# Kernel optimization log

Hardware: AMD Instinct MI355X
Metric: run time of the kernel (lower is better)

Reference implementation:

```python
import jax, jax.numpy as jnp
import numpy as np

N = 10000      # num_nodes
E = 80000      # num_edges
IN = 256       # input_dim
T = 768        # text_embedding_dim
H1, H2 = 1024, 1024
HEADS = 4
ND = 100       # num_domains
NS = 10000     # num_skills
SD = 128       # skill_dim
B = 1024       # skill batch
K = 20         # skills per set
LN_EPS = 1e-5
COS_EPS = 1e-8
NEG_SLOPE = 0.2


def setup_inputs() -> dict:
    key = jax.random.key(0)
    ks = jax.random.split(key, 64)
    r = lambda i, shape, s=0.02: jax.random.normal(ks[i], shape, jnp.float32) * s
    inp = {}
    inp['x'] = jax.random.normal(ks[0], (N, IN), jnp.float32)
    inp['edge_index'] = jax.random.randint(ks[1], (2, E), 0, N)
    inp['domain_ids'] = jax.random.randint(ks[2], (N,), 0, ND)
    inp['skill_ids_1'] = jax.random.randint(ks[3], (B, K), 0, NS)
    inp['skill_ids_2'] = jax.random.randint(ks[4], (B, K), 0, NS)
    for j, name in enumerate(['bio', 'expertise', 'needs', 'goals']):
        inp[name + '_embeddings'] = jax.random.normal(ks[5 + j], (N, T), jnp.float32)
        inp[name + '_w'] = r(9 + 2 * j, (T, T))
        inp[name + '_b'] = jnp.zeros((T,), jnp.float32)
    dims = [IN + 4 * T, H1, H2]
    for i in range(2):
        din, dout = dims[i], dims[i + 1]
        base = 20 + 8 * i
        inp[f'gcn_w{i}'] = r(base, (din, dout))
        inp[f'gcn_b{i}'] = jnp.zeros((dout,), jnp.float32)
        inp[f'gat_w{i}'] = r(base + 1, (dout, dout))
        inp[f'gat_as{i}'] = r(base + 2, (HEADS, dout // HEADS), 0.1)
        inp[f'gat_ad{i}'] = r(base + 3, (HEADS, dout // HEADS), 0.1)
        inp[f'gat_b{i}'] = jnp.zeros((dout,), jnp.float32)
        inp[f'ln_g{i}'] = jnp.ones((dout,), jnp.float32)
        inp[f'ln_b{i}'] = jnp.zeros((dout,), jnp.float32)
    inp['dom_emb'] = r(40, (ND, H2), 1.0)
    inp['dom_w'] = r(41, (H2, H2))
    inp['dom_b'] = jnp.zeros((H2,), jnp.float32)
    inp['skill_emb'] = r(42, (NS, SD), 1.0)
    inp['c_w1'] = r(43, (2 * SD, H2))
    inp['c_b1'] = jnp.zeros((H2,), jnp.float32)
    inp['c_w2'] = r(44, (H2, 1))
    inp['c_b2'] = jnp.zeros((1,), jnp.float32)
    return inp


def _layernorm(x, g, b):
    m = x.mean(-1, keepdims=True)
    v = ((x - m) ** 2).mean(-1, keepdims=True)
    return (x - m) * jax.lax.rsqrt(v + LN_EPS) * g + b


def _gcn(x, src, dst, W, b, n):
    # PyG GCNConv: self loops already in (src,dst); symmetric normalization
    xw = x @ W
    deg = jnp.zeros((n,), x.dtype).at[dst].add(1.0)
    dinv = jax.lax.rsqrt(jnp.maximum(deg, 1.0))  # deg >= 1 due to self loops
    norm = dinv[src] * dinv[dst]                 # [Etot]
    out = jnp.zeros_like(xw).at[dst].add(norm[:, None] * xw[src])
    return out + b


def _gat(x, src, dst, W, a_s, a_d, b, n, heads):
    c = W.shape[1] // heads
    h = (x @ W).reshape(n, heads, c)             # [N,H,C]
    es = jnp.einsum('nhc,hc->nh', h, a_s)
    ed = jnp.einsum('nhc,hc->nh', h, a_d)
    e = jax.nn.leaky_relu(es[src] + ed[dst], NEG_SLOPE)   # [Etot,H]
    m = jnp.full((n, heads), -jnp.inf, x.dtype).at[dst].max(e)
    ee = jnp.exp(e - m[dst])
    s = jnp.zeros((n, heads), x.dtype).at[dst].add(ee)
    alpha = ee / s[dst]                          # segment softmax over dst
    out = jnp.zeros((n, heads, c), x.dtype).at[dst].add(alpha[..., None] * h[src])
    return out.reshape(n, heads * c) + b


def _cos(a, b):
    na = jnp.maximum(jnp.linalg.norm(a, axis=-1), COS_EPS)
    nb = jnp.maximum(jnp.linalg.norm(b, axis=-1), COS_EPS)
    return (a * b).sum(-1) / (na * nb)


def _forward(x, edge_index, domain_ids, skill_ids_1, skill_ids_2,
             bio_embeddings, bio_w, bio_b,
             expertise_embeddings, expertise_w, expertise_b,
             needs_embeddings, needs_w, needs_b,
             goals_embeddings, goals_w, goals_b,
             gcn_w0, gcn_b0, gat_w0, gat_as0, gat_ad0, gat_b0, ln_g0, ln_b0,
             gcn_w1, gcn_b1, gat_w1, gat_as1, gat_ad1, gat_b1, ln_g1, ln_b1,
             dom_emb, dom_w, dom_b, skill_emb, c_w1, c_b1, c_w2, c_b2):
    n = x.shape[0]
    bio_f = bio_embeddings @ bio_w + bio_b
    exp_f = expertise_embeddings @ expertise_w + expertise_b
    needs_f = needs_embeddings @ needs_w + needs_b
    goals_f = goals_embeddings @ goals_w + goals_b
    combined = jnp.concatenate([x, bio_f, exp_f, needs_f, goals_f], axis=1)

    src, dst = edge_index[0], edge_index[1]
    loops = jnp.arange(n)
    srcl = jnp.concatenate([src, loops])   # self loops (GCN & GAT both add them)
    dstl = jnp.concatenate([dst, loops])

    h = combined
    layers = [(gcn_w0, gcn_b0, gat_w0, gat_as0, gat_ad0, gat_b0, ln_g0, ln_b0),
              (gcn_w1, gcn_b1, gat_w1, gat_as1, gat_ad1, gat_b1, ln_g1, ln_b1)]
    for (gw, gb, aw, a_s, a_d, ab, lg, lb) in layers:
        x_gcn = _gcn(h, srcl, dstl, gw, gb, n)
        x_att = _gat(x_gcn, srcl, dstl, aw, a_s, a_d, ab, n, HEADS)
        h = jax.nn.relu(_layernorm(x_att + x_gcn, lg, lb))

    domain_embeddings = h @ dom_w + dom_b + dom_emb[domain_ids]

    s1 = skill_emb[skill_ids_1].mean(axis=1)   # [B,SD]
    s2 = skill_emb[skill_ids_2].mean(axis=1)
    comb = jnp.concatenate([s1, s2], axis=1)
    compat = jax.nn.sigmoid(jax.nn.relu(comb @ c_w1 + c_b1) @ c_w2 + c_b2)

    bio_sim = _cos(bio_f[src], bio_f[dst])
    en_sim = _cos(exp_f[src], needs_f[dst])
    ne_sim = _cos(needs_f[src], exp_f[dst])
    goals_sim = _cos(goals_f[src], goals_f[dst])
    return domain_embeddings, compat, bio_sim, en_sim, ne_sim, goals_sim


def reference(x, edge_index, domain_ids, skill_ids_1, skill_ids_2,
              bio_embeddings, bio_w, bio_b,
              expertise_embeddings, expertise_w, expertise_b,
              needs_embeddings, needs_w, needs_b,
              goals_embeddings, goals_w, goals_b,
              gcn_w0, gcn_b0, gat_w0, gat_as0, gat_ad0, gat_b0, ln_g0, ln_b0,
              gcn_w1, gcn_b1, gat_w1, gat_as1, gat_ad1, gat_b1, ln_g1, ln_b1,
              dom_emb, dom_w, dom_b, skill_emb, c_w1, c_b1, c_w2, c_b2):
    return _forward(x, edge_index, domain_ids, skill_ids_1, skill_ids_2,
                    bio_embeddings, bio_w, bio_b,
                    expertise_embeddings, expertise_w, expertise_b,
                    needs_embeddings, needs_w, needs_b,
                    goals_embeddings, goals_w, goals_b,
                    gcn_w0, gcn_b0, gat_w0, gat_as0, gat_ad0, gat_b0, ln_g0, ln_b0,
                    gcn_w1, gcn_b1, gat_w1, gat_as1, gat_ad1, gat_b1, ln_g1, ln_b1,
                    dom_emb, dom_w, dom_b, skill_emb, c_w1, c_b1, c_w2, c_b2)
```

## Files before the change

kernel.cpp:

```cpp
#include <hip/hip_runtime.h>
#include <math.h>

typedef unsigned short u16;
typedef unsigned short u16x4 __attribute__((ext_vector_type(4)));
typedef unsigned short u16x8 __attribute__((ext_vector_type(8)));
typedef short s16x8 __attribute__((ext_vector_type(8)));
typedef float f32x4 __attribute__((ext_vector_type(4)));

constexpr int NN   = 10000;
constexpr int MP   = 10112;
constexpr int IN   = 256;
constexpr int TD   = 768;
constexpr int CD   = 3328;
constexpr int HD   = 1024;
constexpr int HCH  = 256;
constexpr int SDIM = 128;
constexpr int KSK  = 20;
constexpr int ACAP = 256;
constexpr float LN_EPS = 1e-5f;
constexpr float COS_EPS = 1e-8f;
constexpr float NEG_SLOPE = 0.2f;

__device__ __forceinline__ float warp_sum(float v){
#pragma unroll
  for (int o=1;o<64;o<<=1) v += __shfl_xor(v,o);
  return v;
}
__device__ __forceinline__ float warp_max(float v){
#pragma unroll
  for (int o=1;o<64;o<<=1) v = fmaxf(v, __shfl_xor(v,o));
  return v;
}
__device__ __forceinline__ u16 f2b(float f){
  unsigned u = __float_as_uint(f);
  return (u16)((u + 0x7fffu + ((u>>16)&1u)) >> 16);
}
__device__ __forceinline__ float b2f(u16 b){ return __uint_as_float(((unsigned)b)<<16); }

#define GLDS(g, l) __builtin_amdgcn_global_load_lds( \
    (const __attribute__((address_space(1))) void*)(g), \
    (__attribute__((address_space(3))) void*)(l), 16, 0, 0)

__global__ __launch_bounds__(256) void k_gemm_bf16(
    const u16* __restrict__ A, long Az,
    const u16* __restrict__ B0c, const u16* __restrict__ B1c,
    const u16* __restrict__ B2c, const u16* __restrict__ B3c,
    const float* __restrict__ bias0, const float* __restrict__ bias1,
    const float* __restrict__ bias2, const float* __restrict__ bias3,
    float* __restrict__ Cf, int ldcf,
    u16* __restrict__ Cb, int ldcb, long Cbz,
    const float* __restrict__ demb, const int* __restrict__ dids,
    int M, int K, int relu)
{
  __shared__ __align__(16) u16 smem[16384];
  const int z = blockIdx.z;
  const u16* Bt = (z==0)? B0c : (z==1)? B1c : (z==2)? B2c : B3c;
  const float* bias = (z==0)? bias0 : (z==1)? bias1 : (z==2)? bias2 : bias3;
  const u16* Ab = A + (size_t)z * (size_t)Az;

  const int tid = threadIdx.x;
  const int wave = tid >> 6, lane = tid & 63;
  const int wr = wave >> 1, wc = wave & 1;

  const int nwg  = gridDim.x * gridDim.y;
  const int orig = blockIdx.y * gridDim.x + blockIdx.x;
  const int q = nwg >> 3, r = nwg & 7;
  const int xcd = orig & 7, loc = orig >> 3;
  const int wg = (xcd < r ? xcd*(q+1) : r*(q+1) + (xcd-r)*q) + loc;
  const int bx = wg % gridDim.x, byy = wg / gridDim.x;
  const size_t bm = (size_t)byy * 128;
  const size_t bn = (size_t)bx * 128;

  f32x4 acc[4][4];
#pragma unroll
  for (int m=0;m<4;m++)
#pragma unroll
    for (int n=0;n<4;n++) acc[m][n] = f32x4{0.f,0.f,0.f,0.f};

  const int srow = tid >> 2;
  const int scol = (tid & 3) * 8;
  const u16* ga0 = Ab + (bm + srow) * (size_t)K + scol;
  const u16* ga1 = ga0 + (size_t)64 * K;
  const u16* gb0 = Bt + (bn + srow) * (size_t)K + scol;
  const u16* gb1 = gb0 + (size_t)64 * K;

  auto stage = [&](int buf, int k0){
    GLDS(ga0 + k0, smem + buf*4096 + wave*512);
    GLDS(ga1 + k0, smem + buf*4096 + 2048 + wave*512);
    GLDS(gb0 + k0, smem + 8192 + buf*4096 + wave*512);
    GLDS(gb1 + k0, smem + 8192 + buf*4096 + 2048 + wave*512);
  };

  const int ar = wr*64 + (lane & 15);
  const int br = wc*64 + (lane & 15);
  const int kg = (lane >> 4) * 8;

  const int nt = K >> 5;
  stage(0, 0);
  __syncthreads();
  int cur = 0;
  for (int t = 0; t < nt; ++t){
    if (t+1 < nt) stage(cur^1, (t+1)*32);
    s16x8 a[4], b[4];
#pragma unroll
    for (int m=0;m<4;m++) a[m] = *(const s16x8*)(smem + cur*4096 + (ar + m*16)*32 + kg);
#pragma unroll
    for (int n=0;n<4;n++) b[n] = *(const s16x8*)(smem + 8192 + cur*4096 + (br + n*16)*32 + kg);
#pragma unroll
    for (int m=0;m<4;m++)
#pragma unroll
      for (int n=0;n<4;n++)
        acc[m][n] = __builtin_amdgcn_mfma_f32_16x16x32_bf16(a[m], b[n], acc[m][n], 0, 0, 0);
    __syncthreads();
    cur ^= 1;
  }

  const int cl0 = wc*64 + (lane & 15);
  if (Cb){
#pragma unroll
    for (int m=0;m<4;m++)
#pragma unroll
      for (int j=0;j<4;j++){
        int rl = wr*64 + ((lane >> 4) * 4) + m*16 + j;
#pragma unroll
        for (int n=0;n<4;n++){
          int cl = cl0 + n*16;
          float v = acc[m][n][j];
          if (bias) v += bias[bn + cl];
          if (relu) v = fmaxf(v, 0.f);
          smem[rl*128 + cl] = f2b(v);
        }
      }
    __syncthreads();
#pragma unroll
    for (int it=0; it<8; ++it){
      int rl = it*16 + (tid >> 4);
      int cl = (tid & 15) * 8;
      u16x8 vv = *(const u16x8*)(smem + rl*128 + cl);
      *(u16x8*)(Cb + (size_t)z*Cbz + (bm + rl)*(size_t)ldcb + bn + cl) = vv;
    }
  } else if (Cf){
    float* ctf = (float*)smem;
#pragma unroll
    for (int p=0;p<2;p++){
      if (wr == p){
#pragma unroll
        for (int m=0;m<4;m++)
#pragma unroll
          for (int j=0;j<4;j++){
            int rl = ((lane >> 4) * 4) + m*16 + j;
            int rg = (int)bm + p*64 + rl;
            const float* dbase = (demb && rg < M) ? demb + (size_t)dids[rg]*HD : nullptr;
#pragma unroll
            for (int n=0;n<4;n++){
              int cl = cl0 + n*16;
              float v = acc[m][n][j];
              if (bias) v += bias[bn + cl];
              if (dbase) v += dbase[bn + cl];
              if (relu) v = fmaxf(v, 0.f);
              ctf[rl*128 + cl] = v;
            }
          }
      }
      __syncthreads();
#pragma unroll
      for (int it=0; it<8; ++it){
        int rl = it*8 + (tid >> 5);
        int cl = (tid & 31) * 4;
        int rg = (int)bm + p*64 + rl;
        if (rg < M){
          float4 vv = *(const float4*)(ctf + rl*128 + cl);
          *(float4*)(Cf + (size_t)rg*ldcf + bn + cl) = vv;
        }
      }
      __syncthreads();
    }
  }
}

__global__ void k_f2b8x4(const float* __restrict__ s0, const float* __restrict__ s1,
                         const float* __restrict__ s2, const float* __restrict__ s3,
                         u16* __restrict__ out, long per, long ostride){
  int z = blockIdx.y;
  const float* s = (z==0)? s0 : (z==1)? s1 : (z==2)? s2 : s3;
  long i = ((long)blockIdx.x*256 + threadIdx.x)*8;
  if (i >= per) return;
  float4 v0 = *(const float4*)(s+i);
  float4 v1 = *(const float4*)(s+i+4);
  u16x8 o;
  o[0]=f2b(v0.x); o[1]=f2b(v0.y); o[2]=f2b(v0.z); o[3]=f2b(v0.w);
  o[4]=f2b(v1.x); o[5]=f2b(v1.y); o[6]=f2b(v1.z); o[7]=f2b(v1.w);
  *(u16x8*)(out + z*ostride + i) = o;
}

__global__ void k_copyx_b(const float* __restrict__ x, u16* __restrict__ comb){
  long i = ((long)blockIdx.x*256 + threadIdx.x)*8;
  int n = (int)(i >> 8), c = (int)(i & 255);
  float4 v0 = *(const float4*)(x+i);
  float4 v1 = *(const float4*)(x+i+4);
  u16x8 o;
  o[0]=f2b(v0.x); o[1]=f2b(v0.y); o[2]=f2b(v0.z); o[3]=f2b(v0.w);
  o[4]=f2b(v1.x); o[5]=f2b(v1.y); o[6]=f2b(v1.z); o[7]=f2b(v1.w);
  *(u16x8*)(comb + (size_t)n*CD + c) = o;
}

__global__ __launch_bounds__(256) void k_transb4(
    const float* __restrict__ B0c, const float* __restrict__ B1c,
    const float* __restrict__ B2c, const float* __restrict__ B3c,
    u16* __restrict__ T0, u16* __restrict__ T1,
    u16* __restrict__ T2, u16* __restrict__ T3, int K, int N){
  __shared__ u16 tile[32][40];
  int z = blockIdx.z;
  const float* B = (z==0)? B0c : (z==1)? B1c : (z==2)? B2c : B3c;
  u16* Bt = (z==0)? T0 : (z==1)? T1 : (z==2)? T2 : T3;
  int n0 = blockIdx.x*32, k0 = blockIdx.y*32;
  int tx = threadIdx.x & 31, ty = threadIdx.x >> 5;
#pragma unroll
  for (int i=0;i<4;i++)
    tile[ty+8*i][tx] = f2b(B[(size_t)(k0+ty+8*i)*N + n0+tx]);
  __syncthreads();
#pragma unroll
  for (int i=0;i<4;i++)
    Bt[(size_t)(n0+ty+8*i)*K + k0+tx] = tile[tx][ty+8*i];
}

__global__ void k_hist(const int* __restrict__ dst, int* __restrict__ indeg, int E){
  int e = blockIdx.x*256 + threadIdx.x;
  if (e < E) atomicAdd(&indeg[dst[e]], 1);
}

__global__ __launch_bounds__(1024) void k_scan(const int* __restrict__ indeg,
    int* __restrict__ row_start, int* __restrict__ cursor,
    float* __restrict__ dinv, int Nn)
{
  __shared__ int wsum[16];
  __shared__ int carry_s;
  int t = threadIdx.x, wave = t >> 6, lane = t & 63;
  if (t==0) carry_s = 0;
  __syncthreads();
  for (int base=0; base<Nn; base+=1024) {
    int i = base + t;
    int v = (i<Nn)? indeg[i] : 0;
    int s = v;
#pragma unroll
    for (int o=1;o<64;o<<=1){ int tmp = __shfl_up(s, o); if (lane>=o) s += tmp; }
    if (lane==63) wsum[wave] = s;
    __syncthreads();
    if (wave==0 && lane<16){
      int w = wsum[lane];
#pragma unroll
      for (int o=1;o<16;o<<=1){ int tmp = __shfl_up(w, o); if (lane>=o) w += tmp; }
      wsum[lane] = w;
    }
    __syncthreads();
    int woff = (wave==0)? 0 : wsum[wave-1];
    int incl = s + woff;
    int carry = carry_s;
    if (i<Nn){
      int ex = carry + incl - v;
      row_start[i]=ex; cursor[i]=ex;
      dinv[i] = rsqrtf((float)(v + 1));
    }
    __syncthreads();
    if (t==1023) carry_s = carry + incl;
    __syncthreads();
  }
  if (t==0) row_start[Nn] = carry_s;
}

__global__ void k_scatter(const int* __restrict__ src, const int* __restrict__ dst,
    int* __restrict__ cursor, int* __restrict__ csr_src,
    int* __restrict__ csr_eid, int E){
  int e = blockIdx.x*256 + threadIdx.x;
  if (e < E){
    int d = dst[e];
    int pos = atomicAdd(&cursor[d], 1);
    csr_src[pos] = src[e];
    csr_eid[pos] = e;
  }
}

__global__ __launch_bounds__(128) void k_gcn_agg(
    const u16* __restrict__ xw, const int* __restrict__ row_start,
    const int* __restrict__ csr_src, const float* __restrict__ dinv,
    const float* __restrict__ bias, u16* __restrict__ outb)
{
  int d = blockIdx.x, t = threadIdx.x;
  int c0 = t*8;
  float di = dinv[d];
  u16x8 sv = *(const u16x8*)(xw + (size_t)d*HD + c0);
  float acc[8];
#pragma unroll
  for (int i=0;i<8;i++) acc[i] = di*di*b2f(sv[i]);
  int beg = row_start[d], end = row_start[d+1];
  int j = beg;
  for (; j+4 <= end; j += 4){
    int s0=csr_src[j], s1=csr_src[j+1], s2=csr_src[j+2], s3=csr_src[j+3];
    u16x8 r0 = *(const u16x8*)(xw + (size_t)s0*HD + c0);
    u16x8 r1 = *(const u16x8*)(xw + (size_t)s1*HD + c0);
    u16x8 r2 = *(const u16x8*)(xw + (size_t)s2*HD + c0);
    u16x8 r3 = *(const u16x8*)(xw + (size_t)s3*HD + c0);
    float w0=di*dinv[s0], w1=di*dinv[s1], w2=di*dinv[s2], w3=di*dinv[s3];
#pragma unroll
    for (int i=0;i<8;i++){
      acc[i] = fmaf(w0, b2f(r0[i]), acc[i]);
      acc[i] = fmaf(w1, b2f(r1[i]), acc[i]);
      acc[i] = fmaf(w2, b2f(r2[i]), acc[i]);
      acc[i] = fmaf(w3, b2f(r3[i]), acc[i]);
    }
  }
  for (; j<end; ++j){
    int s = csr_src[j];
    float w = di*dinv[s];
    u16x8 rv = *(const u16x8*)(xw + (size_t)s*HD + c0);
#pragma unroll
    for (int i=0;i<8;i++) acc[i] = fmaf(w, b2f(rv[i]), acc[i]);
  }
  float4 bv0 = *(const float4*)(bias + c0);
  float4 bv1 = *(const float4*)(bias + c0 + 4);
  float o[8] = {acc[0]+bv0.x, acc[1]+bv0.y, acc[2]+bv0.z, acc[3]+bv0.w,
                acc[4]+bv1.x, acc[5]+bv1.y, acc[6]+bv1.z, acc[7]+bv1.w};
  u16x8 ob;
#pragma unroll
  for (int i=0;i<8;i++) ob[i]=f2b(o[i]);
  *(u16x8*)(outb + (size_t)d*HD + c0) = ob;
}

__global__ __launch_bounds__(256) void k_es_ed(
    const u16* __restrict__ hw, const float* __restrict__ a_s,
    const float* __restrict__ a_d, float* __restrict__ es, float* __restrict__ ed)
{
  int n = blockIdx.x; int wv = threadIdx.x >> 6; int lane = threadIdx.x & 63;
  u16x4 v  = *(const u16x4*)(hw + (size_t)n*HD + wv*HCH + lane*4);
  float4 as = *(const float4*)(a_s + wv*HCH + lane*4);
  float4 ad = *(const float4*)(a_d + wv*HCH + lane*4);
  float f0=b2f(v[0]), f1=b2f(v[1]), f2v=b2f(v[2]), f3=b2f(v[3]);
  float ss = f0*as.x + f1*as.y + f2v*as.z + f3*as.w;
  float sd = f0*ad.x + f1*ad.y + f2v*ad.z + f3*ad.w;
  ss = warp_sum(ss); sd = warp_sum(sd);
  if (lane==0){ es[n*4+wv]=ss; ed[n*4+wv]=sd; }
}

__global__ __launch_bounds__(128) void k_gat_fused(
    const u16* __restrict__ hw, const int* __restrict__ row_start,
    const int* __restrict__ csr_src, const float* __restrict__ es,
    const float* __restrict__ ed, const float* __restrict__ bias,
    const u16* __restrict__ gcn, const float* __restrict__ g,
    const float* __restrict__ b, u16* __restrict__ out)
{
  __shared__ float4 alph[ACAP];
  __shared__ float xch[8];
  int d = blockIdx.x, t = threadIdx.x, wv = t>>6, lane = t&63;
  int beg = row_start[d], end = row_start[d+1], deg = end-beg;
  float4 edq = *(const float4*)(ed + (size_t)d*4);
  float4 esq = *(const float4*)(es + (size_t)d*4);
  float edv[4] = {edq.x,edq.y,edq.z,edq.w};
  float esv[4] = {esq.x,esq.y,esq.z,esq.w};
  float eself[4], m[4];
#pragma unroll
  for (int h=0;h<4;h++){
    float e = esv[h] + edv[h];
    eself[h] = (e>0.f)? e : NEG_SLOPE*e;
    m[h] = eself[h];
  }
  for (int j=beg+t; j<end; j+=128){
    int s = csr_src[j];
    float4 qv = *(const float4*)(es + (size_t)s*4);
    float qa[4] = {qv.x,qv.y,qv.z,qv.w};
#pragma unroll
    for (int h=0;h<4;h++){
      float e = qa[h]+edv[h]; e = (e>0.f)? e : NEG_SLOPE*e;
      m[h] = fmaxf(m[h], e);
    }
  }
#pragma unroll
  for (int h=0;h<4;h++) m[h] = warp_max(m[h]);
  if (lane==0) ((float4*)xch)[wv] = make_float4(m[0],m[1],m[2],m[3]);
  __syncthreads();
  {
    float4 m0 = ((float4*)xch)[0], m1 = ((float4*)xch)[1];
    m[0]=fmaxf(m0.x,m1.x); m[1]=fmaxf(m0.y,m1.y);
    m[2]=fmaxf(m0.z,m1.z); m[3]=fmaxf(m0.w,m1.w);
  }
  __syncthreads();
  bool fits = (deg <= ACAP);
  float sum[4] = {0.f,0.f,0.f,0.f};
  for (int j=beg+t; j<end; j+=128){
    int s = csr_src[j];
    float4 qv = *(const float4*)(es + (size_t)s*4);
    float qa[4] = {qv.x,qv.y,qv.z,qv.w}, p[4];
#pragma unroll
    for (int h=0;h<4;h++){
      float e = qa[h]+edv[h]; e = (e>0.f)? e : NEG_SLOPE*e;
      p[h] = expf(e-m[h]); sum[h]+=p[h];
    }
    if (fits) alph[j-beg] = make_float4(p[0],p[1],p[2],p[3]);
  }
#pragma unroll
  for (int h=0;h<4;h++) sum[h]=warp_sum(sum[h]);
  if (lane==0) ((float4*)xch)[wv] = make_float4(sum[0],sum[1],sum[2],sum[3]);
  __syncthreads();
  float rsm[4], swt[4];
  {
    float4 s0=((float4*)xch)[0], s1=((float4*)xch)[1];
    float sa[4] = {s0.x+s1.x, s0.y+s1.y, s0.z+s1.z, s0.w+s1.w};
#pragma unroll
    for (int h=0;h<4;h++){
      float pe = expf(eself[h]-m[h]);
      rsm[h] = 1.f/(sa[h]+pe);
      swt[h] = pe*rsm[h];
    }
  }
  int c0 = t*8, h0 = t>>5;
  u16x8 sv = *(const u16x8*)(hw + (size_t)d*HD + c0);
  float acc[8];
#pragma unroll
  for (int i=0;i<8;i++) acc[i] = swt[h0]*b2f(sv[i]);
  float mh = m[h0], rh = rsm[h0], edh = edv[h0];
  if (fits){
    int j = beg;
    for (; j+4 <= end; j += 4){
      int s0=csr_src[j], s1=csr_src[j+1], s2=csr_src[j+2], s3=csr_src[j+3];
      u16x8 r0 = *(const u16x8*)(hw + (size_t)s0*HD + c0);
      u16x8 r1 = *(const u16x8*)(hw + (size_t)s1*HD + c0);
      u16x8 r2 = *(const u16x8*)(hw + (size_t)s2*HD + c0);
      u16x8 r3 = *(const u16x8*)(hw + (size_t)s3*HD + c0);
      float a0 = ((const float*)&alph[j-beg  ])[h0] * rh;
      float a1 = ((const float*)&alph[j-beg+1])[h0] * rh;
      float a2 = ((const float*)&alph[j-beg+2])[h0] * rh;
      float a3 = ((const float*)&alph[j-beg+3])[h0] * rh;
#pragma unroll
      for (int i=0;i<8;i++){
        acc[i] = fmaf(a0, b2f(r0[i]), acc[i]);
        acc[i] = fmaf(a1, b2f(r1[i]), acc[i]);
        acc[i] = fmaf(a2, b2f(r2[i]), acc[i]);
        acc[i] = fmaf(a3, b2f(r3[i]), acc[i]);
      }
    }
    for (; j<end; ++j){
      int s = csr_src[j];
      float av = ((const float*)&alph[j-beg])[h0] * rh;
      u16x8 rv = *(const u16x8*)(hw + (size_t)s*HD + c0);
#pragma unroll
      for (int i=0;i<8;i++) acc[i] = fmaf(av, b2f(rv[i]), acc[i]);
    }
  } else {
    for (int j=beg; j<end; ++j){
      int s = csr_src[j];
      float e = es[(size_t)s*4+h0] + edh; e = (e>0.f)? e : NEG_SLOPE*e;
      float av = expf(e-mh)*rh;
      u16x8 rv = *(const u16x8*)(hw + (size_t)s*HD + c0);
#pragma unroll
      for (int i=0;i<8;i++) acc[i] = fmaf(av, b2f(rv[i]), acc[i]);
    }
  }
  float4 bv0 = *(const float4*)(bias + c0), bv1 = *(const float4*)(bias + c0 + 4);
  u16x8 gv = *(const u16x8*)(gcn + (size_t)d*HD + c0);
  float ba8[8] = {bv0.x,bv0.y,bv0.z,bv0.w,bv1.x,bv1.y,bv1.z,bv1.w};
  float xv[8];
#pragma unroll
  for (int i=0;i<8;i++) xv[i] = acc[i] + ba8[i] + b2f(gv[i]);
  float ssum=0.f, ssq=0.f;
#pragma unroll
  for (int i=0;i<8;i++){ ssum += xv[i]; ssq = fmaf(xv[i], xv[i], ssq); }
  ssum = warp_sum(ssum); ssq = warp_sum(ssq);
  __syncthreads();
  if (lane==0){ xch[wv]=ssum; xch[2+wv]=ssq; }
  __syncthreads();
  ssum = xch[0]+xch[1]; ssq = xch[2]+xch[3];
  float mean = ssum * (1.f/HD);
  float var  = ssq * (1.f/HD) - mean*mean;
  float rsln = rsqrtf(var + LN_EPS);
  float4 gg0 = *(const float4*)(g + c0), gg1 = *(const float4*)(g + c0 + 4);
  float4 bb0 = *(const float4*)(b + c0), bb1 = *(const float4*)(b + c0 + 4);
  float ga[8] = {gg0.x,gg0.y,gg0.z,gg0.w,gg1.x,gg1.y,gg1.z,gg1.w};
  float ba[8] = {bb0.x,bb0.y,bb0.z,bb0.w,bb1.x,bb1.y,bb1.z,bb1.w};
  u16x8 ob;
#pragma unroll
  for (int i=0;i<8;i++)
    ob[i] = f2b(fmaxf((xv[i]-mean)*rsln*ga[i] + ba[i], 0.f));
  *(u16x8*)(out + (size_t)d*HD + c0) = ob;
}

__global__ __launch_bounds__(256) void k_norms_b(const u16* __restrict__ comb,
                                                 float* __restrict__ norms)
{
  int n = blockIdx.x; int wv = threadIdx.x>>6, lane = threadIdx.x&63;
  const int base[4] = {IN, IN+TD, IN+2*TD, IN+3*TD};
  const u16* a = comb + (size_t)n*CD + base[wv];
  float ss=0.f;
  for (int j=lane*8; j<TD; j+=512){
    u16x8 v = *(const u16x8*)(a+j);
#pragma unroll
    for (int k=0;k<8;k++){ float f = b2f(v[k]); ss = fmaf(f,f,ss); }
  }
  ss = warp_sum(ss);
  if (lane==0) norms[n*4+wv] = sqrtf(ss);
}

__global__ __launch_bounds__(256) void k_sims_csr(
    const u16* __restrict__ comb, const float* __restrict__ norms,
    const int* __restrict__ row_start, const int* __restrict__ csr_src,
    const int* __restrict__ csr_eid, float* __restrict__ out, int E)
{
  int d = blockIdx.x;
  int w = threadIdx.x>>6, lane = threadIdx.x&63;
  int g = lane>>4, l = lane&15;
  int beg = row_start[d], end = row_start[d+1];
  if (beg >= end) return;
  const int baseA[4] = {IN, IN+TD,   IN+2*TD, IN+3*TD};
  const int baseB[4] = {IN, IN+2*TD, IN+TD,   IN+3*TD};
  const int nA[4] = {0,1,2,3}, nB[4] = {0,2,1,3};
  const u16* bp = comb + (size_t)d*CD + baseB[g] + l*8;
  float bf[48];
#pragma unroll
  for (int i=0;i<6;i++){
    u16x8 v = *(const u16x8*)(bp + i*128);
#pragma unroll
    for (int k=0;k<8;k++) bf[i*8+k] = b2f(v[k]);
  }
  float rnb = 1.f / fmaxf(norms[(size_t)d*4+nB[g]], COS_EPS);
  for (int j = beg + w; j < end; j += 4){
    int s = csr_src[j];
    const u16* ap = comb + (size_t)s*CD + baseA[g] + l*8;
    float dot = 0.f;
#pragma unroll
    for (int i=0;i<6;i++){
      u16x8 v = *(const u16x8*)(ap + i*128);
#pragma unroll
      for (int k=0;k<8;k++) dot = fmaf(b2f(v[k]), bf[i*8+k], dot);
    }
    dot += __shfl_xor(dot,1); dot += __shfl_xor(dot,2);
    dot += __shfl_xor(dot,4); dot += __shfl_xor(dot,8);
    if (l==0){
      float na = fmaxf(norms[(size_t)s*4+nA[g]], COS_EPS);
      out[(size_t)g*E + csr_eid[j]] = dot * rnb / na;
    }
  }
}

__global__ __launch_bounds__(128) void k_skill_mean_b(
    const float* __restrict__ semb, const int* __restrict__ id1,
    const int* __restrict__ id2, u16* __restrict__ comb)
{
  int b = blockIdx.x, c = threadIdx.x;
  float s1=0.f, s2=0.f;
  for (int k=0;k<KSK;k++){
    s1 += semb[(size_t)id1[b*KSK+k]*SDIM + c];
    s2 += semb[(size_t)id2[b*KSK+k]*SDIM + c];
  }
  comb[(size_t)b*256 + c]       = f2b(s1*(1.f/KSK));
  comb[(size_t)b*256 + 128 + c] = f2b(s2*(1.f/KSK));
}

__global__ __launch_bounds__(256) void k_compat(
    const float* __restrict__ hidden, const float* __restrict__ w2,
    const float* __restrict__ b2, float* __restrict__ out)
{
  __shared__ float red[4];
  int bi = blockIdx.x, t = threadIdx.x;
  float s = 0.f;
  for (int c=t;c<HD;c+=256) s = fmaf(hidden[(size_t)bi*HD+c], w2[c], s);
  s = warp_sum(s);
  if ((t&63)==0) red[t>>6] = s;
  __syncthreads();
  if (t==0){
    float tot = red[0]+red[1]+red[2]+red[3] + b2[0];
    out[bi] = 1.f/(1.f+expf(-tot));
  }
}

extern "C" void kernel_launch(void* const* d_in, const int* in_sizes, int n_in,
                              void* d_out, int out_size, void* d_ws, size_t ws_size,
                              hipStream_t stream)
{
  const float* x         = (const float*)d_in[0];
  const int*   eidx      = (const int*)d_in[1];
  const int*   dom_ids   = (const int*)d_in[2];
  const int*   sk1       = (const int*)d_in[3];
  const int*   sk2       = (const int*)d_in[4];
  const float* bio_emb   = (const float*)d_in[5];
  const float* bio_w     = (const float*)d_in[6];
  const float* bio_b     = (const float*)d_in[7];
  const float* exp_emb   = (const float*)d_in[8];
  const float* exp_w     = (const float*)d_in[9];
  const float* exp_b     = (const float*)d_in[10];
  const float* needs_emb = (const float*)d_in[11];
  const float* needs_w   = (const float*)d_in[12];
  const float* needs_b   = (const float*)d_in[13];
  const float* goals_emb = (const float*)d_in[14];
  const float* goals_w   = (const float*)d_in[15];
  const float* goals_b   = (const float*)d_in[16];
  const float* gcn_w0 = (const float*)d_in[17];
  const float* gcn_b0 = (const float*)d_in[18];
  const float* gat_w0 = (const float*)d_in[19];
  const float* gat_as0= (const float*)d_in[20];
  const float* gat_ad0= (const float*)d_in[21];
  const float* gat_b0 = (const float*)d_in[22];
  const float* ln_g0  = (const float*)d_in[23];
  const float* ln_b0  = (const float*)d_in[24];
  const float* gcn_w1 = (const float*)d_in[25];
  const float* gcn_b1 = (const float*)d_in[26];
  const float* gat_w1 = (const float*)d_in[27];
  const float* gat_as1= (const float*)d_in[28];
  const float* gat_ad1= (const float*)d_in[29];
  const float* gat_b1 = (const float*)d_in[30];
  const float* ln_g1  = (const float*)d_in[31];
  const float* ln_b1  = (const float*)d_in[32];
  const float* dom_emb= (const float*)d_in[33];
  const float* dom_w  = (const float*)d_in[34];
  const float* dom_b  = (const float*)d_in[35];
  const float* skill_emb = (const float*)d_in[36];
  const float* c_w1   = (const float*)d_in[37];
  const float* c_b1   = (const float*)d_in[38];
  const float* c_w2   = (const float*)d_in[39];
  const float* c_b2   = (const float*)d_in[40];

  const int E   = in_sizes[1] / 2;
  const int Bsz = in_sizes[3] / KSK;
  const int* srcp = eidx;
  const int* dstp = eidx + E;

  char* wsp = (char*)d_ws;
  size_t off = 0;
  auto alloc = [&](size_t bytes)->void*{
    void* p = wsp + off;
    off += (bytes + 255) & ~(size_t)255;
    return p;
  };
  u16*   combined_b = (u16*)alloc((size_t)MP*CD*2);
  u16*   Aact       = (u16*)alloc((size_t)4*MP*TD*2);
  u16*   P0b  = (u16*) alloc((size_t)MP*HD*2);
  u16*   P1b  = (u16*) alloc((size_t)MP*HD*2);
  u16*   Rh   = (u16*) alloc((size_t)MP*HD*2);
  u16*   wt_bio   = (u16*)alloc((size_t)TD*TD*2);
  u16*   wt_exp   = (u16*)alloc((size_t)TD*TD*2);
  u16*   wt_needs = (u16*)alloc((size_t)TD*TD*2);
  u16*   wt_goals = (u16*)alloc((size_t)TD*TD*2);
  u16*   w_gcn0t  = (u16*)alloc((size_t)HD*CD*2);
  u16*   w_gat0t  = (u16*)alloc((size_t)HD*HD*2);
  u16*   w_gcn1t  = (u16*)alloc((size_t)HD*HD*2);
  u16*   w_gat1t  = (u16*)alloc((size_t)HD*HD*2);
  u16*   w_domt   = (u16*)alloc((size_t)HD*HD*2);
  u16*   w_c1t    = (u16*)alloc((size_t)HD*2*SDIM*2);
  u16*   comb_b   = (u16*)alloc((size_t)Bsz*2*SDIM*2);
  float* hidden   = (float*)alloc((size_t)Bsz*HD*4);
  float* es      = (float*)alloc((size_t)NN*4*4);
  float* ed      = (float*)alloc((size_t)NN*4*4);
  float* dinv    = (float*)alloc((size_t)NN*4);
  int*   indeg   = (int*)  alloc((size_t)NN*4);
  int*   row_st  = (int*)  alloc((size_t)(NN+1)*4);
  int*   cursor  = (int*)  alloc((size_t)NN*4);
  int*   csr_src = (int*)  alloc((size_t)E*4);
  int*   csr_eid = (int*)  alloc((size_t)E*4);
  float* norms   = (float*)alloc((size_t)NN*4*4);

  u16* Rhwb = combined_b;

  float* out0       = (float*)d_out;
  float* out_compat = out0 + (size_t)NN*HD;
  float* out_sims   = out_compat + Bsz;

  dim3 blk(256);

  hipMemsetAsync(indeg, 0, (size_t)NN*sizeof(int), stream);
  k_hist<<<dim3((E+255)/256), blk, 0, stream>>>(dstp, indeg, E);
  k_scan<<<dim3(1), dim3(1024), 0, stream>>>(indeg, row_st, cursor, dinv, NN);
  k_scatter<<<dim3((E+255)/256), blk, 0, stream>>>(srcp, dstp, cursor, csr_src, csr_eid, E);

  k_transb4<<<dim3(TD/32, TD/32, 4), blk, 0, stream>>>(
      bio_w, exp_w, needs_w, goals_w, wt_bio, wt_exp, wt_needs, wt_goals, TD, TD);
  k_transb4<<<dim3(HD/32, HD/32, 4), blk, 0, stream>>>(
      gat_w0, gcn_w1, gat_w1, dom_w, w_gat0t, w_gcn1t, w_gat1t, w_domt, HD, HD);
  k_transb4<<<dim3(HD/32, CD/32, 1), blk, 0, stream>>>(
      gcn_w0, gcn_w0, gcn_w0, gcn_w0, w_gcn0t, w_gcn0t, w_gcn0t, w_gcn0t, CD, HD);
  k_transb4<<<dim3(HD/32, (2*SDIM)/32, 1), blk, 0, stream>>>(
      c_w1, c_w1, c_w1, c_w1, w_c1t, w_c1t, w_c1t, w_c1t, 2*SDIM, HD);

  k_copyx_b<<<dim3((NN*IN)/8/256), blk, 0, stream>>>(x, combined_b);
  k_f2b8x4<<<dim3((NN*TD)/8/256, 4), blk, 0, stream>>>(
      bio_emb, exp_emb, needs_emb, goals_emb, Aact, (long)NN*TD, (long)MP*TD);
  k_gemm_bf16<<<dim3(TD/128, MP/128, 4), blk, 0, stream>>>(
      Aact, (long)MP*TD, wt_bio, wt_exp, wt_needs, wt_goals,
      bio_b, exp_b, needs_b, goals_b,
      nullptr, 0, combined_b + IN, CD, (long)TD,
      nullptr, nullptr, NN, TD, 0);

  k_norms_b<<<dim3(NN), blk, 0, stream>>>(combined_b, norms);
  k_sims_csr<<<dim3(NN), blk, 0, stream>>>(combined_b, norms, row_st, csr_src,
                                           csr_eid, out_sims, E);

  k_skill_mean_b<<<dim3(Bsz), dim3(128), 0, stream>>>(skill_emb, sk1, sk2, comb_b);
  k_gemm_bf16<<<dim3(HD/128, Bsz/128, 1), blk, 0, stream>>>(
      comb_b, 0, w_c1t, w_c1t, w_c1t, w_c1t, c_b1, c_b1, c_b1, c_b1,
      hidden, HD, nullptr, 0, 0, nullptr, nullptr, Bsz, 2*SDIM, 1);
  k_compat<<<dim3(Bsz), blk, 0, stream>>>(hidden, c_w2, c_b2, out_compat);

  dim3 g_h(HD/128, MP/128, 1);

  k_gemm_bf16<<<g_h, blk, 0, stream>>>(
      combined_b, 0, w_gcn0t, w_gcn0t, w_gcn0t, w_gcn0t,
      nullptr, nullptr, nullptr, nullptr,
      nullptr, 0, P0b, HD, 0, nullptr, nullptr, NN, CD, 0);
  k_gcn_agg<<<dim3(NN), dim3(128), 0, stream>>>(P0b, row_st, csr_src, dinv, gcn_b0, P1b);
  k_gemm_bf16<<<g_h, blk, 0, stream>>>(
      P1b, 0, w_gat0t, w_gat0t, w_gat0t, w_gat0t,
      nullptr, nullptr, nullptr, nullptr,
      nullptr, 0, Rhwb, HD, 0, nullptr, nullptr, NN, HD, 0);
  k_es_ed<<<dim3(NN), blk, 0, stream>>>(Rhwb, gat_as0, gat_ad0, es, ed);
  k_gat_fused<<<dim3(NN), dim3(128), 0, stream>>>(Rhwb, row_st, csr_src, es, ed,
                                                  gat_b0, P1b, ln_g0, ln_b0, Rh);

  k_gemm_bf16<<<g_h, blk, 0, stream>>>(
      Rh, 0, w_gcn1t, w_gcn1t, w_gcn1t, w_gcn1t,
      nullptr, nullptr, nullptr, nullptr,
      nullptr, 0, P0b, HD, 0, nullptr, nullptr, NN, HD, 0);
  k_gcn_agg<<<dim3(NN), dim3(128), 0, stream>>>(P0b, row_st, csr_src, dinv, gcn_b1, P1b);
  k_gemm_bf16<<<g_h, blk, 0, stream>>>(
      P1b, 0, w_gat1t, w_gat1t, w_gat1t, w_gat1t,
      nullptr, nullptr, nullptr, nullptr,
      nullptr, 0, Rhwb, HD, 0, nullptr, nullptr, NN, HD, 0);
  k_es_ed<<<dim3(NN), blk, 0, stream>>>(Rhwb, gat_as1, gat_ad1, es, ed);
  k_gat_fused<<<dim3(NN), dim3(128), 0, stream>>>(Rhwb, row_st, csr_src, es, ed,
                                                  gat_b1, P1b, ln_g1, ln_b1, Rh);

  k_gemm_bf16<<<g_h, blk, 0, stream>>>(
      Rh, 0, w_domt, w_domt, w_domt, w_domt,
      dom_b, dom_b, dom_b, dom_b,
      out0, HD, nullptr, 0, 0, dom_emb, dom_ids, NN, HD, 0);
}
```

Before: 656.5 us.

## Add 256x256-tile bf16 MFMA GEMM with XCD remapping and staged pipelining

Adds a new 512-thread GEMM kernel with 256x256 output tiles, 16x16x32 bf16 MFMA, double-buffered direct global-to-LDS loads interleaved with compute phases, s_setprio hints, and an XCD-aware workgroup remap. All large node GEMMs switch to it, and the padded row count rises to a multiple of 256. The larger tiles are meant to improve operand reuse and cut global traffic relative to the 128x128 kernel. In exchange the grid has fewer blocks, each using 128KB of LDS and heavy registers, which may lower occupancy and leave the grid unevenly spread across CUs.

New measurement: 712.6 us. +8.5%, slower.

```diff
diff --git a/kernel.cpp b/kernel.cpp
--- a/kernel.cpp
+++ b/kernel.cpp
@@ -8,7 +8,7 @@
 typedef float f32x4 __attribute__((ext_vector_type(4)));
 
 constexpr int NN   = 10000;
-constexpr int MP   = 10112;
+constexpr int MP   = 10240;
 constexpr int IN   = 256;
 constexpr int TD   = 768;
 constexpr int CD   = 3328;
@@ -40,6 +40,218 @@
 #define GLDS(g, l) __builtin_amdgcn_global_load_lds( \
     (const __attribute__((address_space(1))) void*)(g), \
     (__attribute__((address_space(3))) void*)(l), 16, 0, 0)
+
+#define MFMA16(a,b,c) __builtin_amdgcn_mfma_f32_16x16x32_bf16((a),(b),(c),0,0,0)
+
+__global__ __launch_bounds__(512, 2) void k_gemm256(
+    const u16* __restrict__ A, long Az,
+    const u16* __restrict__ B0c, const u16* __restrict__ B1c,
+    const u16* __restrict__ B2c, const u16* __restrict__ B3c,
+    const float* __restrict__ bias0, const float* __restrict__ bias1,
+    const float* __restrict__ bias2, const float* __restrict__ bias3,
+    float* __restrict__ Cf, int ldcf,
+    u16* __restrict__ Cb, int ldcb, long Cbz,
+    const float* __restrict__ demb, const int* __restrict__ dids,
+    int M, int K, int relu)
+{
+  __shared__ __align__(16) u16 smem[65536];
+  const int z = blockIdx.z;
+  const u16* Bt = (z==0)? B0c : (z==1)? B1c : (z==2)? B2c : B3c;
+  const float* bias = (z==0)? bias0 : (z==1)? bias1 : (z==2)? bias2 : bias3;
+  const u16* Ab = A + (size_t)z * (size_t)Az;
+
+  const int tid  = threadIdx.x;
+  const int wave = tid >> 6, lane = tid & 63;
+  const int wr = wave >> 2, wc = wave & 3;
+  const int lr = lane & 15;
+
+  const int nwg  = gridDim.x * gridDim.y;
+  const int orig = blockIdx.y * gridDim.x + blockIdx.x;
+  const int q = nwg >> 3, r = nwg & 7;
+  const int xcd = orig & 7, loc = orig >> 3;
+  const int wg = (xcd < r ? xcd*(q+1) : r*(q+1) + (xcd-r)*q) + loc;
+  const int bx = wg % gridDim.x, byy = wg / gridDim.x;
+  const size_t bm = (size_t)byy * 256;
+  const size_t bn = (size_t)bx * 256;
+
+  const int kx0 = ((lane>>4)<<3) ^ ((lane&7)<<3);
+  const int kx1 = kx0 ^ 32;
+
+  const int rt  = tid >> 3;
+  const int sl8 = (((tid&7) ^ (rt&7))) << 3;
+
+  const int nt  = K >> 6;
+  const int nt4 = nt << 2;
+
+  f32x4 acc[8][4];
+#pragma unroll
+  for (int m=0;m<8;m++)
+#pragma unroll
+    for (int n=0;n<4;n++) acc[m][n] = f32x4{0.f,0.f,0.f,0.f};
+
+  auto stage = [&](int H){
+    if (H >= nt4) return;
+    const int j = H & 3;
+    const long k0 = (long)(H >> 2) << 6;
+    const u16* g = (j < 2)
+      ? Ab + (bm + (size_t)(j*128 + rt)) * (size_t)K + k0 + sl8
+      : Bt + (bn + (size_t)((j-2)*128 + rt)) * (size_t)K + k0 + sl8;
+    u16* l = smem + ((H>>2)&1)*32768 + j*8192 + wave*512;
+    GLDS(g, l);
+    GLDS(g + (size_t)64*K, l + 4096);
+  };
+
+  stage(0); stage(1); stage(2); stage(3); stage(4);
+  asm volatile("s_waitcnt vmcnt(2)" ::: "memory");
+  __builtin_amdgcn_s_barrier();
+
+  for (int t = 0; t < nt; ++t){
+    const u16* lA = smem + (t&1)*32768 + wr*8192;
+    const u16* lB = smem + (t&1)*32768 + (2 + (wc>>1))*8192 + (wc&1)*4096;
+    s16x8 a[4][2], b0[2][2], b1[2][2];
+#pragma unroll
+    for (int m=0;m<4;m++){
+      int ro = (m*16 + lr)*64;
+      a[m][0] = *(const s16x8*)(lA + ro + kx0);
+      a[m][1] = *(const s16x8*)(lA + ro + kx1);
+    }
+#pragma unroll
+    for (int n=0;n<2;n++){
+      int ro = (n*16 + lr)*64;
+      b0[n][0] = *(const s16x8*)(lB + ro + kx0);
+      b0[n][1] = *(const s16x8*)(lB + ro + kx1);
+    }
+    stage(4*t + 5);
+    __builtin_amdgcn_s_barrier();
+    asm volatile("s_waitcnt lgkmcnt(0)" ::: "memory");
+    __builtin_amdgcn_s_setprio(1);
+#pragma unroll
+    for (int m=0;m<4;m++)
+#pragma unroll
+      for (int n=0;n<2;n++){
+        acc[m][n] = MFMA16(a[m][0], b0[n][0], acc[m][n]);
+        acc[m][n] = MFMA16(a[m][1], b0[n][1], acc[m][n]);
+      }
+    __builtin_amdgcn_s_setprio(0);
+    __builtin_amdgcn_s_barrier();
+#pragma unroll
+    for (int n=0;n<2;n++){
+      int ro = ((n+2)*16 + lr)*64;
+      b1[n][0] = *(const s16x8*)(lB + ro + kx0);
+      b1[n][1] = *(const s16x8*)(lB + ro + kx1);
+    }
+    stage(4*t + 6);
+    __builtin_amdgcn_s_barrier();
+    asm volatile("s_waitcnt lgkmcnt(0)" ::: "memory");
+    __builtin_amdgcn_s_setprio(1);
+#pragma unroll
+    for (int m=0;m<4;m++)
+#pragma unroll
+      for (int n=0;n<2;n++){
+        acc[m][n+2] = MFMA16(a[m][0], b1[n][0], acc[m][n+2]);
+        acc[m][n+2] = MFMA16(a[m][1], b1[n][1], acc[m][n+2]);
+      }
+    __builtin_amdgcn_s_setprio(0);
+    __builtin_amdgcn_s_barrier();
+#pragma unroll
+    for (int m=0;m<4;m++){
+      int ro = ((m+4)*16 + lr)*64;
+      a[m][0] = *(const s16x8*)(lA + ro + kx0);
+      a[m][1] = *(const s16x8*)(lA + ro + kx1);
+    }
+    stage(4*t + 7);
+    __builtin_amdgcn_s_barrier();
+    asm volatile("s_waitcnt lgkmcnt(0)" ::: "memory");
+    __builtin_amdgcn_s_setprio(1);
+#pragma unroll
+    for (int m=0;m<4;m++)
+#pragma unroll
+      for (int n=0;n<2;n++){
+        acc[m+4][n+2] = MFMA16(a[m][0], b1[n][0], acc[m+4][n+2]);
+        acc[m+4][n+2] = MFMA16(a[m][1], b1[n][1], acc[m+4][n+2]);
+      }
+    __builtin_amdgcn_s_setprio(0);
+    __builtin_amdgcn_s_barrier();
+    stage(4*t + 8);
+    __builtin_amdgcn_s_barrier();
+    __builtin_amdgcn_s_setprio(1);
+#pragma unroll
+    for (int m=0;m<4;m++)
+#pragma unroll
+      for (int n=0;n<2;n++){
+        acc[m+4][n] = MFMA16(a[m][0], b0[n][0], acc[m+4][n]);
+        acc[m+4][n] = MFMA16(a[m][1], b0[n][1], acc[m+4][n]);
+      }
+    __builtin_amdgcn_s_setprio(0);
+    if (t < nt-2) asm volatile("s_waitcnt vmcnt(2)" ::: "memory");
+    else          asm volatile("s_waitcnt vmcnt(0)" ::: "memory");
+    __builtin_amdgcn_s_barrier();
+  }
+  __syncthreads();
+
+  if (Cb){
+    u16* ct = smem;
+#pragma unroll
+    for (int m=0;m<8;m++)
+#pragma unroll
+      for (int j=0;j<4;j++){
+        int rl = wr*128 + m*16 + ((lane>>4)<<2) + j;
+#pragma unroll
+        for (int n=0;n<4;n++){
+          int cl = wc*64 + n*16 + lr;
+          float v = acc[m][n][j];
+          if (bias) v += bias[bn + cl];
+          if (relu) v = fmaxf(v, 0.f);
+          ct[rl*256 + cl] = f2b(v);
+        }
+      }
+    __syncthreads();
+#pragma unroll
+    for (int it=0; it<16; ++it){
+      int rl = it*16 + (tid >> 5);
+      int cl = (tid & 31) * 8;
+      u16x8 vv = *(const u16x8*)(ct + rl*256 + cl);
+      *(u16x8*)(Cb + (size_t)z*Cbz + (bm + rl)*(size_t)ldcb + bn + cl) = vv;
+    }
+  } else if (Cf){
+    float* ctf = (float*)smem;
+#pragma unroll
+    for (int p=0;p<2;p++){
+      if (wr == p){
+#pragma unroll
+        for (int m=0;m<8;m++)
+#pragma unroll
+          for (int j=0;j<4;j++){
+            int rl = m*16 + ((lane>>4)<<2) + j;
+            size_t rg = bm + (size_t)p*128 + rl;
+            const float* dbase = (demb && rg < (size_t)M)
+                               ? demb + (size_t)dids[rg]*(size_t)ldcf : nullptr;
+#pragma unroll
+            for (int n=0;n<4;n++){
+              int cl = wc*64 + n*16 + lr;
+              float v = acc[m][n][j];
+              if (bias)  v += bias[bn + cl];
+              if (dbase) v += dbase[bn + cl];
+              if (relu)  v = fmaxf(v, 0.f);
+              ctf[rl*256 + cl] = v;
+            }
+          }
+      }
+      __syncthreads();
+#pragma unroll
+      for (int it=0; it<16; ++it){
+        int rl = it*8 + (tid >> 6);
+        int cl = (tid & 63) * 4;
+        size_t rg = bm + (size_t)p*128 + rl;
+        if (rg < (size_t)M){
+          float4 vv = *(const float4*)(ctf + rl*256 + cl);
+          *(float4*)(Cf + rg*(size_t)ldcf + bn + cl) = vv;
+        }
+      }
+      __syncthreads();
+    }
+  }
+}
 
 __global__ __launch_bounds__(256) void k_gemm_bf16(
     const u16* __restrict__ A, long Az,
@@ -662,6 +874,7 @@
   float* out_sims   = out_compat + Bsz;
 
   dim3 blk(256);
+  dim3 blk512(512);
 
   hipMemsetAsync(indeg, 0, (size_t)NN*sizeof(int), stream);
   k_hist<<<dim3((E+255)/256), blk, 0, stream>>>(dstp, indeg, E);
@@ -680,7 +893,7 @@
   k_copyx_b<<<dim3((NN*IN)/8/256), blk, 0, stream>>>(x, combined_b);
   k_f2b8x4<<<dim3((NN*TD)/8/256, 4), blk, 0, stream>>>(
       bio_emb, exp_emb, needs_emb, goals_emb, Aact, (long)NN*TD, (long)MP*TD);
-  k_gemm_bf16<<<dim3(TD/128, MP/128, 4), blk, 0, stream>>>(
+  k_gemm256<<<dim3(TD/256, MP/256, 4), blk512, 0, stream>>>(
       Aact, (long)MP*TD, wt_bio, wt_exp, wt_needs, wt_goals,
       bio_b, exp_b, needs_b, goals_b,
       nullptr, 0, combined_b + IN, CD, (long)TD,
@@ -696,14 +909,14 @@
       hidden, HD, nullptr, 0, 0, nullptr, nullptr, Bsz, 2*SDIM, 1);
   k_compat<<<dim3(Bsz), blk, 0, stream>>>(hidden, c_w2, c_b2, out_compat);
 
-  dim3 g_h(HD/128, MP/128, 1);
-
-  k_gemm_bf16<<<g_h, blk, 0, stream>>>(
+  dim3 g_h256(HD/256, MP/256, 1);
+
+  k_gemm256<<<g_h256, blk512, 0, stream>>>(
       combined_b, 0, w_gcn0t, w_gcn0t, w_gcn0t, w_gcn0t,
       nullptr, nullptr, nullptr, nullptr,
       nullptr, 0, P0b, HD, 0, nullptr, nullptr, NN, CD, 0);
   k_gcn_agg<<<dim3(NN), dim3(128), 0, stream>>>(P0b, row_st, csr_src, dinv, gcn_b0, P1b);
-  k_gemm_bf16<<<g_h, blk, 0, stream>>>(
+  k_gemm256<<<g_h256, blk512, 0, stream>>>(
       P1b, 0, w_gat0t, w_gat0t, w_gat0t, w_gat0t,
       nullptr, nullptr, nullptr, nullptr,
       nullptr, 0, Rhwb, HD, 0, nullptr, nullptr, NN, HD, 0);
@@ -711,12 +924,12 @@
   k_gat_fused<<<dim3(NN), dim3(128), 0, stream>>>(Rhwb, row_st, csr_src, es, ed,
                                                   gat_b0, P1b, ln_g0, ln_b0, Rh);
 
-  k_gemm_bf16<<<g_h, blk, 0, stream>>>(
+  k_gemm256<<<g_h256, blk512, 0, stream>>>(
       Rh, 0, w_gcn1t, w_gcn1t, w_gcn1t, w_gcn1t,
       nullptr, nullptr, nullptr, nullptr,
       nullptr, 0, P0b, HD, 0, nullptr, nullptr, NN, HD, 0);
   k_gcn_agg<<<dim3(NN), dim3(128), 0, stream>>>(P0b, row_st, csr_src, dinv, gcn_b1, P1b);
-  k_gemm_bf16<<<g_h, blk, 0, stream>>>(
+  k_gemm256<<<g_h256, blk512, 0, stream>>>(
       P1b, 0, w_gat1t, w_gat1t, w_gat1t, w_gat1t,
       nullptr, nullptr, nullptr, nullptr,
       nullptr, 0, Rhwb, HD, 0, nullptr, nullptr, NN, HD, 0);
@@ -724,7 +937,7 @@
   k_gat_fused<<<dim3(NN), dim3(128), 0, stream>>>(Rhwb, row_st, csr_src, es, ed,
                                                   gat_b1, P1b, ln_g1, ln_b1, Rh);
 
-  k_gemm_bf16<<<g_h, blk, 0, stream>>>(
+  k_gemm256<<<g_h256, blk512, 0, stream>>>(
       Rh, 0, w_domt, w_domt, w_domt, w_domt,
       dom_b, dom_b, dom_b, dom_b,
       out0, HD, nullptr, 0, 0, dom_emb, dom_ids, NN, HD, 0);
```
